# Kernel tuning notes

Measured on AMD Instinct MI355X. Metric: run time of the kernel, lower is better.

## Reference

```python
import jax, jax.numpy as jnp
import numpy as np

B, Tq, DIM = 4, 2048, 1024
TKV, N_LAT, DLAT = 16, 64, 1024
HEADS, DHEAD = 8, 64
LN_EPS = 1e-5


def setup_inputs() -> dict:
    key = jax.random.key(0)
    ks = jax.random.split(key, 6)
    qo = jax.random.normal(ks[0], (B, Tq, DIM), dtype=jnp.float32)
    kvo = jax.random.normal(ks[1], (B, TKV, N_LAT, DLAT), dtype=jnp.float32)
    # 16 media tokens, evenly spaced, first at index 16 (so q_time==0 for early tokens)
    media = jnp.zeros((B, Tq), dtype=bool)
    idx = 16 + jnp.arange(TKV) * (Tq // TKV)  # 16, 144, ..., 1936
    media = media.at[:, idx].set(True)
    ln_g = jnp.ones((DIM,), dtype=jnp.float32)
    ln_b = jnp.zeros((DIM,), dtype=jnp.float32)
    Wq = jax.random.normal(ks[2], (DIM, HEADS * DHEAD), dtype=jnp.float32) * 0.02
    Wkv = jax.random.normal(ks[3], (DLAT, HEADS * DHEAD * 2), dtype=jnp.float32) * 0.02
    Wout = jax.random.normal(ks[4], (HEADS * DHEAD, DIM), dtype=jnp.float32) * 0.02
    return {"qo": qo, "kvo": kvo, "media_locations": media,
            "ln_g": ln_g, "ln_b": ln_b, "Wq": Wq, "Wkv": Wkv, "Wout": Wout}


def _layernorm(x, g, b):
    mu = jnp.mean(x, axis=-1, keepdims=True)
    var = jnp.var(x, axis=-1, keepdims=True)
    return (x - mu) * jax.lax.rsqrt(var + LN_EPS) * g + b


def reference(qo, kvo, media_locations, ln_g, ln_b, Wq, Wkv, Wout):
    scale = DHEAD ** (-0.5)
    b, tq, _ = qo.shape
    _, tkv, n, _ = kvo.shape
    q = _layernorm(qo, ln_g, ln_b) @ Wq  # (b, tq, h*d)
    q = q.reshape(b, tq, HEADS, DHEAD).transpose(0, 2, 1, 3) * scale  # b h i d
    kv = kvo.reshape(b, tkv * n, -1) @ Wkv  # (b, j, 2*h*d)
    k, v = jnp.split(kv, 2, axis=-1)
    k = k.reshape(b, tkv * n, HEADS, DHEAD).transpose(0, 2, 1, 3)  # b h j d
    v = v.reshape(b, tkv * n, HEADS, DHEAD).transpose(0, 2, 1, 3)
    sim = jnp.einsum('bhid,bhjd->bhij', q, k)  # (b, h, tq, tkv*n)
    kv_time = jnp.repeat(jnp.arange(tkv) + 1, n)  # (tkv*n,)
    q_time = jnp.cumsum(media_locations.astype(jnp.int32), axis=-1)  # (b, tq)
    mask = q_time[:, None, :, None] == kv_time[None, None, None, :]  # only_attend_immediate
    neg = -jnp.finfo(sim.dtype).max
    sim = jnp.where(mask, sim, neg)
    attn = jax.nn.softmax(sim, axis=-1)
    attn = jnp.where((q_time == 0)[:, None, :, None], 0.0, attn)
    out = jnp.einsum('bhij,bhjd->bhid', attn, v)
    out = out.transpose(0, 2, 1, 3).reshape(b, tq, HEADS * DHEAD)
    return out @ Wout
```

## Files before the change

### kernel.cpp

```cpp
#include <hip/hip_runtime.h>
#include <cstdint>
#include <cstddef>

#define BB    4
#define TQ    2048
#define DIM   1024
#define TKV   16
#define NLAT  64
#define DLAT  1024
#define HEADS 8
#define DHEAD 64
#define LN_EPS 1e-5f
#define NKV   (TKV*NLAT)
#define HD    (HEADS*DHEAD)

typedef unsigned short u16;
typedef __bf16 bf16x8 __attribute__((ext_vector_type(8)));
typedef float  f32x4  __attribute__((ext_vector_type(4)));

__device__ __forceinline__ u16 f2bf(float f) {
    unsigned u = __builtin_bit_cast(unsigned, f);
    u += 0x7fffu + ((u >> 16) & 1u);
    return (u16)(u >> 16);
}
__device__ __forceinline__ void gl_lds16(const void* g, void* l) {
    __builtin_amdgcn_global_load_lds(
        (const __attribute__((address_space(1))) void*)g,
        (__attribute__((address_space(3))) void*)l, 16, 0, 0);
}

__device__ __forceinline__ void transpose_dev(const float* __restrict__ W,
                                              u16* __restrict__ Wt,
                                              int K, int N, int n0, int k0,
                                              float (*tile)[33]) {
    int t = threadIdx.x;
    int r = t >> 3, c4 = (t & 7) * 4;
    float4 v = *(const float4*)&W[(size_t)(k0 + r) * N + n0 + c4];
    tile[r][c4 + 0] = v.x; tile[r][c4 + 1] = v.y;
    tile[r][c4 + 2] = v.z; tile[r][c4 + 3] = v.w;
    __syncthreads();
    uint2 pk;
    pk.x = (unsigned)f2bf(tile[c4 + 0][r]) | ((unsigned)f2bf(tile[c4 + 1][r]) << 16);
    pk.y = (unsigned)f2bf(tile[c4 + 2][r]) | ((unsigned)f2bf(tile[c4 + 3][r]) << 16);
    *(uint2*)&Wt[(size_t)(n0 + r) * K + k0 + c4] = pk;
}

__global__ __launch_bounds__(256) void prep_k(
    const float* __restrict__ qo, const float* __restrict__ kvo,
    const uint8_t* __restrict__ media,
    const float* __restrict__ ln_g, const float* __restrict__ ln_b,
    const float* __restrict__ Wq, const float* __restrict__ Wkv,
    const float* __restrict__ Wout,
    int* __restrict__ qt, u16* __restrict__ Aq, u16* __restrict__ Akv,
    u16* __restrict__ Wqt, u16* __restrict__ Wkvt, u16* __restrict__ Woutt) {
    __shared__ int part[256];
    __shared__ int cnt_sh;
    __shared__ float sh[8];
    __shared__ float mu_s, rs_s;
    __shared__ float tile[32][33];
    int blk = blockIdx.x, t = threadIdx.x;

    if (blk < 4) {
        int b = blk;
        int c = 0;
        for (int i = 0; i < 32; ++i) c += (media[t * 32 + i] != 0);
        part[t] = c;
        __syncthreads();
        if (t == 0) { int s = 0; for (int i = 0; i < 256; ++i) s += part[i]; cnt_sh = s; }
        __syncthreads();
        bool is_u8 = (cnt_sh >= 48);
        int vals[8];
        for (int i = 0; i < 8; ++i) {
            int idx = t * 8 + i;
            int m;
            if (is_u8) m = (media[(size_t)b * TQ + idx] != 0) ? 1 : 0;
            else       m = (((const uint32_t*)media)[(size_t)b * TQ + idx] != 0u) ? 1 : 0;
            vals[i] = m;
        }
        int loc = 0;
        for (int i = 0; i < 8; ++i) loc += vals[i];
        __syncthreads();
        part[t] = loc;
        __syncthreads();
        int pre = 0;
        for (int i = 0; i < t; ++i) pre += part[i];
        int run = pre;
        for (int i = 0; i < 8; ++i) {
            run += vals[i];
            qt[(size_t)b * TQ + t * 8 + i] = run;
        }
    } else if (blk < 4 + BB * TQ) {
        int row = blk - 4;
        float4 v = *(const float4*)(qo + (size_t)row * DIM + t * 4);
        float s  = v.x + v.y + v.z + v.w;
        float ss = v.x * v.x + v.y * v.y + v.z * v.z + v.w * v.w;
        for (int off = 32; off; off >>= 1) { s += __shfl_down(s, off); ss += __shfl_down(ss, off); }
        if ((t & 63) == 0) { sh[(t >> 6) * 2] = s; sh[(t >> 6) * 2 + 1] = ss; }
        __syncthreads();
        if (t == 0) {
            float S  = sh[0] + sh[2] + sh[4] + sh[6];
            float SS = sh[1] + sh[3] + sh[5] + sh[7];
            float m  = S * (1.0f / DIM);
            mu_s = m;
            rs_s = rsqrtf(SS * (1.0f / DIM) - m * m + LN_EPS);
        }
        __syncthreads();
        float mu = mu_s, rs = rs_s;
        float4 gv = *(const float4*)(ln_g + t * 4);
        float4 bv = *(const float4*)(ln_b + t * 4);
        float a0 = (v.x - mu) * rs * gv.x + bv.x;
        float a1 = (v.y - mu) * rs * gv.y + bv.y;
        float a2 = (v.z - mu) * rs * gv.z + bv.z;
        float a3 = (v.w - mu) * rs * gv.w + bv.w;
        uint2 pk;
        pk.x = (unsigned)f2bf(a0) | ((unsigned)f2bf(a1) << 16);
        pk.y = (unsigned)f2bf(a2) | ((unsigned)f2bf(a3) << 16);
        *(uint2*)(Aq + (size_t)row * DIM + t * 4) = pk;
    } else if (blk < 4 + BB * TQ + 2048) {
        size_t i = (size_t)(blk - 4 - BB * TQ) * 256 + t;
        float4 a = ((const float4*)kvo)[i * 2];
        float4 b = ((const float4*)kvo)[i * 2 + 1];
        uint4 pk;
        pk.x = (unsigned)f2bf(a.x) | ((unsigned)f2bf(a.y) << 16);
        pk.y = (unsigned)f2bf(a.z) | ((unsigned)f2bf(a.w) << 16);
        pk.z = (unsigned)f2bf(b.x) | ((unsigned)f2bf(b.y) << 16);
        pk.w = (unsigned)f2bf(b.z) | ((unsigned)f2bf(b.w) << 16);
        ((uint4*)Akv)[i] = pk;
    } else if (blk < 10244 + 512) {
        int id = blk - 10244;
        transpose_dev(Wq, Wqt, DIM, HD, (id & 15) * 32, (id >> 4) * 32, tile);
    } else if (blk < 10756 + 1024) {
        int id = blk - 10756;
        transpose_dev(Wkv, Wkvt, DLAT, 2 * HD, (id & 31) * 32, (id >> 5) * 32, tile);
    } else {
        int id = blk - 11780;
        transpose_dev(Wout, Woutt, HD, DIM, (id & 31) * 32, (id >> 5) * 32, tile);
    }
}

template <typename CT>
__device__ __forceinline__ void gemm_body(const u16* __restrict__ A,
                                          const u16* __restrict__ Bt,
                                          CT* __restrict__ C,
                                          int M, int N, int K, float outscale,
                                          int bx, int by,
                                          u16* As0, u16* Bs0, u16* As1, u16* Bs1) {
    int t = threadIdx.x;
    int lane = t & 63, w = t >> 6;
    int wr = w >> 1, wc = w & 1;
    int fr = lane & 15, fg = lane >> 4;
    int row0 = by * 128, col0 = bx * 128;

    const u16* Ag = A  + (size_t)(row0 + (t >> 2)) * K + (t & 3) * 8;
    const u16* Bg = Bt + (size_t)(col0 + (t >> 2)) * K + (t & 3) * 8;
    size_t rstr = (size_t)64 * K;

    int aoff = (wr * 64 + fr) * 32 + fg * 8;
    int boff = (wc * 64 + fr) * 32 + fg * 8;

    f32x4 acc[4][4];
#pragma unroll
    for (int mi = 0; mi < 4; ++mi)
#pragma unroll
        for (int ni = 0; ni < 4; ++ni) acc[mi][ni] = (f32x4){0.f, 0.f, 0.f, 0.f};

    auto stage = [&](u16* Asb, u16* Bsb, int k0) {
        char* al = (char*)Asb + w * 1024;
        char* bl = (char*)Bsb + w * 1024;
        gl_lds16(Ag + k0,        al);
        gl_lds16(Ag + k0 + rstr, al + 4096);
        gl_lds16(Bg + k0,        bl);
        gl_lds16(Bg + k0 + rstr, bl + 4096);
    };
    auto compute = [&](const u16* Asb, const u16* Bsb) {
        bf16x8 af[4], bfv[4];
#pragma unroll
        for (int mi = 0; mi < 4; ++mi) af[mi]  = *(const bf16x8*)(Asb + aoff + mi * 512);
#pragma unroll
        for (int ni = 0; ni < 4; ++ni) bfv[ni] = *(const bf16x8*)(Bsb + boff + ni * 512);
#pragma unroll
        for (int mi = 0; mi < 4; ++mi)
#pragma unroll
            for (int ni = 0; ni < 4; ++ni)
                acc[mi][ni] = __builtin_amdgcn_mfma_f32_16x16x32_bf16(
                    af[mi], bfv[ni], acc[mi][ni], 0, 0, 0);
    };

    int nt = K >> 5;
    stage(As0, Bs0, 0);
    __syncthreads();
    for (int it = 0; it < nt; it += 2) {
        stage(As1, Bs1, (it + 1) << 5);
        compute(As0, Bs0);
        __syncthreads();
        if (it + 2 < nt) stage(As0, Bs0, (it + 2) << 5);
        compute(As1, Bs1);
        __syncthreads();
    }

#pragma unroll
    for (int mi = 0; mi < 4; ++mi) {
        int r0 = row0 + wr * 64 + mi * 16 + fg * 4;
#pragma unroll
        for (int ni = 0; ni < 4; ++ni) {
            int c = col0 + wc * 64 + ni * 16 + fr;
#pragma unroll
            for (int j = 0; j < 4; ++j) {
                float val = acc[mi][ni][j] * outscale;
                if constexpr (sizeof(CT) == 2) C[(size_t)(r0 + j) * N + c] = f2bf(val);
                else                           C[(size_t)(r0 + j) * N + c] = val;
            }
        }
    }
}

__global__ __launch_bounds__(256) void proj_k(
    const u16* __restrict__ Aq,  const u16* __restrict__ Wqt,  u16* __restrict__ qb,
    const u16* __restrict__ Akv, const u16* __restrict__ Wkvt, u16* __restrict__ kvb) {
    __shared__ u16 As0[4096], Bs0[4096], As1[4096], Bs1[4096];
    int id = blockIdx.x;
    if (id < 256) {
        gemm_body<u16>(Aq, Wqt, qb, BB * TQ, HD, DIM, 0.125f, id & 3, id >> 2,
                       As0, Bs0, As1, Bs1);
    } else {
        id -= 256;
        gemm_body<u16>(Akv, Wkvt, kvb, BB * NKV, 2 * HD, DLAT, 1.0f, id & 7, id >> 3,
                       As0, Bs0, As1, Bs1);
    }
}

__global__ __launch_bounds__(256) void out_k(
    const u16* __restrict__ aob, const u16* __restrict__ Woutt, float* __restrict__ out) {
    __shared__ u16 As0[4096], Bs0[4096], As1[4096], Bs1[4096];
    int id = blockIdx.x;
    gemm_body<float>(aob, Woutt, out, BB * TQ, DIM, HD, 1.0f, id & 7, id >> 3,
                     As0, Bs0, As1, Bs1);
}

__global__ __launch_bounds__(256) void attn_k(
    const u16* __restrict__ q,
    const u16* __restrict__ kv,
    const int* __restrict__ qt,
    u16* __restrict__ ao) {
    __shared__ u16 Ks[4096];
    __shared__ u16 VT[4096];
    __shared__ u16 Ps[1024];
    __shared__ float redm[4][16], reds[4][16];
    int i0 = blockIdx.x * 16;
    int h  = blockIdx.y;
    int b  = blockIdx.z;
    int t  = threadIdx.x;
    int lane = t & 63, w = t >> 6;
    int fr = lane & 15, fg = lane >> 4;

    int t0 = qt[(size_t)b * TQ + i0];
    if (t0 == 0) {
        int row = t >> 4, c = (t & 15) * 4;
        *(uint2*)&ao[((size_t)(b * TQ + i0 + row)) * HD + h * DHEAD + c] = make_uint2(0, 0);
        return;
    }
    int j0 = (t0 - 1) * 64;

    {
        int j = t >> 2, c16 = (t & 3) * 16;
        const u16* kvrow = kv + ((size_t)(b * NKV + j0 + j)) * (2 * HD) + h * DHEAD;
        uint4 k0v = *(const uint4*)(kvrow + c16);
        uint4 k1v = *(const uint4*)(kvrow + c16 + 8);
        uint4 v0v = *(const uint4*)(kvrow + HD + c16);
        uint4 v1v = *(const uint4*)(kvrow + HD + c16 + 8);
        int kb = j * 128 + c16 * 2;
        int swz = (j & 7) << 4;
        *(uint4*)((char*)Ks + ((kb)      ^ swz)) = k0v;
        *(uint4*)((char*)Ks + ((kb + 16) ^ swz)) = k1v;
        const u16* ve0 = (const u16*)&v0v;
        const u16* ve1 = (const u16*)&v1v;
#pragma unroll
        for (int e = 0; e < 8; ++e) {
            int d0 = c16 + e, d1 = c16 + 8 + e;
            *(u16*)((char*)VT + ((d0 * 128 + j * 2) ^ ((d0 & 7) << 4))) = ve0[e];
            *(u16*)((char*)VT + ((d1 * 128 + j * 2) ^ ((d1 & 7) << 4))) = ve1[e];
        }
    }
    const u16* qrow = q + ((size_t)(b * TQ + i0 + fr)) * HD + h * DHEAD + fg * 8;
    bf16x8 aq0 = *(const bf16x8*)(qrow);
    bf16x8 aq1 = *(const bf16x8*)(qrow + 32);
    __syncthreads();

    int r = w * 16 + fr;
    bf16x8 bk0 = *(const bf16x8*)((char*)Ks + ((r * 128 + fg * 16)      ^ ((r & 7) << 4)));
    bf16x8 bk1 = *(const bf16x8*)((char*)Ks + ((r * 128 + 64 + fg * 16) ^ ((r & 7) << 4)));
    f32x4 s = (f32x4){0.f, 0.f, 0.f, 0.f};
    s = __builtin_amdgcn_mfma_f32_16x16x32_bf16(aq0, bk0, s, 0, 0, 0);
    s = __builtin_amdgcn_mfma_f32_16x16x32_bf16(aq1, bk1, s, 0, 0, 0);

    float mx[4];
#pragma unroll
    for (int j = 0; j < 4; ++j) {
        float m = s[j];
        for (int off = 1; off < 16; off <<= 1) m = fmaxf(m, __shfl_xor(m, off));
        mx[j] = m;
        redm[w][fg * 4 + j] = m;
    }
    __syncthreads();
    float p[4];
#pragma unroll
    for (int j = 0; j < 4; ++j) {
        int row = fg * 4 + j;
        float M = fmaxf(fmaxf(redm[0][row], redm[1][row]), fmaxf(redm[2][row], redm[3][row]));
        p[j] = __expf(s[j] - M);
        float sm = p[j];
        for (int off = 1; off < 16; off <<= 1) sm += __shfl_xor(sm, off);
        reds[w][row] = sm;
    }
    __syncthreads();
#pragma unroll
    for (int j = 0; j < 4; ++j) {
        int row = fg * 4 + j;
        float S = reds[0][row] + reds[1][row] + reds[2][row] + reds[3][row];
        u16 pb = f2bf(p[j] / S);
        *(u16*)((char*)Ps + ((row * 128 + (w * 16 + fr) * 2) ^ ((row & 7) << 4))) = pb;
    }
    __syncthreads();

    bf16x8 pa0 = *(const bf16x8*)((char*)Ps + ((fr * 128 + fg * 16)      ^ ((fr & 7) << 4)));
    bf16x8 pa1 = *(const bf16x8*)((char*)Ps + ((fr * 128 + 64 + fg * 16) ^ ((fr & 7) << 4)));
    int d = w * 16 + fr;
    bf16x8 bv0 = *(const bf16x8*)((char*)VT + ((d * 128 + fg * 16)      ^ ((d & 7) << 4)));
    bf16x8 bv1 = *(const bf16x8*)((char*)VT + ((d * 128 + 64 + fg * 16) ^ ((d & 7) << 4)));
    f32x4 o = (f32x4){0.f, 0.f, 0.f, 0.f};
    o = __builtin_amdgcn_mfma_f32_16x16x32_bf16(pa0, bv0, o, 0, 0, 0);
    o = __builtin_amdgcn_mfma_f32_16x16x32_bf16(pa1, bv1, o, 0, 0, 0);
#pragma unroll
    for (int j = 0; j < 4; ++j)
        ao[((size_t)(b * TQ + i0 + fg * 4 + j)) * HD + h * DHEAD + d] = f2bf(o[j]);
}

extern "C" void kernel_launch(void* const* d_in, const int* in_sizes, int n_in,
                              void* d_out, int out_size, void* d_ws, size_t ws_size,
                              hipStream_t stream) {
    const float*   qo    = (const float*)d_in[0];
    const float*   kvo   = (const float*)d_in[1];
    const uint8_t* media = (const uint8_t*)d_in[2];
    const float*   ln_g  = (const float*)d_in[3];
    const float*   ln_b  = (const float*)d_in[4];
    const float*   Wq    = (const float*)d_in[5];
    const float*   Wkv   = (const float*)d_in[6];
    const float*   Wout  = (const float*)d_in[7];
    float* out = (float*)d_out;

    char* ws = (char*)d_ws;
    const size_t MB = 1u << 20;
    int* qt    = (int*)(ws);
    u16* Aq    = (u16*)(ws + 1  * MB);
    u16* aob   = (u16*)(ws + 1  * MB);
    u16* Akv   = (u16*)(ws + 17 * MB);
    u16* Wqt   = (u16*)(ws + 25 * MB);
    u16* Wkvt  = (u16*)(ws + 26 * MB);
    u16* Woutt = (u16*)(ws + 28 * MB);
    u16* qb    = (u16*)(ws + 29 * MB);
    u16* kvb   = (u16*)(ws + 37 * MB);

    prep_k<<<dim3(12292), dim3(256), 0, stream>>>(qo, kvo, media, ln_g, ln_b,
                                                  Wq, Wkv, Wout,
                                                  qt, Aq, Akv, Wqt, Wkvt, Woutt);
    proj_k<<<dim3(512), dim3(256), 0, stream>>>(Aq, Wqt, qb, Akv, Wkvt, kvb);
    attn_k<<<dim3(TQ / 16, HEADS, BB), dim3(256), 0, stream>>>(qb, kvb, qt, aob);
    out_k<<<dim3(512), dim3(256), 0, stream>>>(aob, Woutt, out);
}
```

Measured before the change: 169.8 us.

## Pre-swizzle GEMM operands in global memory and widen K-tile to 64

The producers of the GEMM operands (LN output, kvo bf16 copy, transposed weights, attention output) now write each row in 16-byte chunks XOR-swizzled by row. The GEMM can then copy a 64-wide K tile straight into LDS with global_load_lds and read it without bank conflicts. The K step doubles, so each barrier pair covers twice the MFMA work and LDS use doubles to 64KB per block. The cost is coupling every producer to the swizzle layout and lower occupancy from the larger LDS footprint.

```diff
diff --git a/kernel.cpp b/kernel.cpp
--- a/kernel.cpp
+++ b/kernel.cpp
@@ -28,6 +28,9 @@
         (const __attribute__((address_space(1))) void*)g,
         (__attribute__((address_space(3))) void*)l, 16, 0, 0);
 }
+__device__ __forceinline__ int swz_idx(int col, int row) {
+    return (col & ~63) | ((((col >> 3) & 7) ^ (row & 7)) << 3) | (col & 7);
+}
 
 __device__ __forceinline__ void transpose_dev(const float* __restrict__ W,
                                               u16* __restrict__ Wt,
@@ -42,7 +45,8 @@
     uint2 pk;
     pk.x = (unsigned)f2bf(tile[c4 + 0][r]) | ((unsigned)f2bf(tile[c4 + 1][r]) << 16);
     pk.y = (unsigned)f2bf(tile[c4 + 2][r]) | ((unsigned)f2bf(tile[c4 + 3][r]) << 16);
-    *(uint2*)&Wt[(size_t)(n0 + r) * K + k0 + c4] = pk;
+    int n = n0 + r, k = k0 + c4;
+    *(uint2*)&Wt[(size_t)n * K + swz_idx(k, n)] = pk;
 }
 
 __global__ __launch_bounds__(256) void prep_k(
@@ -115,7 +119,7 @@
         uint2 pk;
         pk.x = (unsigned)f2bf(a0) | ((unsigned)f2bf(a1) << 16);
         pk.y = (unsigned)f2bf(a2) | ((unsigned)f2bf(a3) << 16);
-        *(uint2*)(Aq + (size_t)row * DIM + t * 4) = pk;
+        *(uint2*)(Aq + (size_t)row * DIM + swz_idx(t * 4, row)) = pk;
     } else if (blk < 4 + BB * TQ + 2048) {
         size_t i = (size_t)(blk - 4 - BB * TQ) * 256 + t;
         float4 a = ((const float4*)kvo)[i * 2];
@@ -125,7 +129,9 @@
         pk.y = (unsigned)f2bf(a.z) | ((unsigned)f2bf(a.w) << 16);
         pk.z = (unsigned)f2bf(b.x) | ((unsigned)f2bf(b.y) << 16);
         pk.w = (unsigned)f2bf(b.z) | ((unsigned)f2bf(b.w) << 16);
-        ((uint4*)Akv)[i] = pk;
+        int row = (int)(i >> 7);
+        size_t di = (i & ~(size_t)7) | (size_t)(((int)i & 7) ^ (row & 7));
+        ((uint4*)Akv)[di] = pk;
     } else if (blk < 10244 + 512) {
         int id = blk - 10244;
         transpose_dev(Wq, Wqt, DIM, HD, (id & 15) * 32, (id >> 4) * 32, tile);
@@ -139,9 +145,7 @@
 }
 
 template <typename CT>
-__device__ __forceinline__ void gemm_body(const u16* __restrict__ A,
-                                          const u16* __restrict__ Bt,
-                                          CT* __restrict__ C,
+__device__ __forceinline__ void gemm_body(const u16* A, const u16* Bt, CT* C,
                                           int M, int N, int K, float outscale,
                                           int bx, int by,
                                           u16* As0, u16* Bs0, u16* As1, u16* Bs1) {
@@ -150,13 +154,11 @@
     int wr = w >> 1, wc = w & 1;
     int fr = lane & 15, fg = lane >> 4;
     int row0 = by * 128, col0 = bx * 128;
-
-    const u16* Ag = A  + (size_t)(row0 + (t >> 2)) * K + (t & 3) * 8;
-    const u16* Bg = Bt + (size_t)(col0 + (t >> 2)) * K + (t & 3) * 8;
-    size_t rstr = (size_t)64 * K;
-
-    int aoff = (wr * 64 + fr) * 32 + fg * 8;
-    int boff = (wc * 64 + fr) * 32 + fg * 8;
+    int swz = fr & 7;
+
+    const u16* Ag = A  + (size_t)(row0 + w * 32 + (lane >> 3)) * K + (lane & 7) * 8;
+    const u16* Bg = Bt + (size_t)(col0 + w * 32 + (lane >> 3)) * K + (lane & 7) * 8;
+    size_t i8K = (size_t)8 * K;
 
     f32x4 acc[4][4];
 #pragma unroll
@@ -164,36 +166,43 @@
 #pragma unroll
         for (int ni = 0; ni < 4; ++ni) acc[mi][ni] = (f32x4){0.f, 0.f, 0.f, 0.f};
 
-    auto stage = [&](u16* Asb, u16* Bsb, int k0) {
-        char* al = (char*)Asb + w * 1024;
-        char* bl = (char*)Bsb + w * 1024;
-        gl_lds16(Ag + k0,        al);
-        gl_lds16(Ag + k0 + rstr, al + 4096);
-        gl_lds16(Bg + k0,        bl);
-        gl_lds16(Bg + k0 + rstr, bl + 4096);
+    auto stage = [&](u16* Asb, u16* Bsb, int kt) {
+        int k0 = kt << 6;
+#pragma unroll
+        for (int q = 0; q < 4; ++q) {
+            gl_lds16(Ag + k0 + q * i8K, (char*)Asb + w * 4096 + q * 1024);
+            gl_lds16(Bg + k0 + q * i8K, (char*)Bsb + w * 4096 + q * 1024);
+        }
     };
     auto compute = [&](const u16* Asb, const u16* Bsb) {
-        bf16x8 af[4], bfv[4];
-#pragma unroll
-        for (int mi = 0; mi < 4; ++mi) af[mi]  = *(const bf16x8*)(Asb + aoff + mi * 512);
-#pragma unroll
-        for (int ni = 0; ni < 4; ++ni) bfv[ni] = *(const bf16x8*)(Bsb + boff + ni * 512);
-#pragma unroll
-        for (int mi = 0; mi < 4; ++mi)
+#pragma unroll
+        for (int ks = 0; ks < 2; ++ks) {
+            bf16x8 af[4], bfv[4];
+#pragma unroll
+            for (int mi = 0; mi < 4; ++mi)
+                af[mi] = *(const bf16x8*)((const char*)Asb +
+                    (wr * 64 + mi * 16 + fr) * 128 + (((ks * 4 + fg) ^ swz) << 4));
 #pragma unroll
             for (int ni = 0; ni < 4; ++ni)
-                acc[mi][ni] = __builtin_amdgcn_mfma_f32_16x16x32_bf16(
-                    af[mi], bfv[ni], acc[mi][ni], 0, 0, 0);
+                bfv[ni] = *(const bf16x8*)((const char*)Bsb +
+                    (wc * 64 + ni * 16 + fr) * 128 + (((ks * 4 + fg) ^ swz) << 4));
+#pragma unroll
+            for (int mi = 0; mi < 4; ++mi)
+#pragma unroll
+                for (int ni = 0; ni < 4; ++ni)
+                    acc[mi][ni] = __builtin_amdgcn_mfma_f32_16x16x32_bf16(
+                        af[mi], bfv[ni], acc[mi][ni], 0, 0, 0);
+        }
     };
 
-    int nt = K >> 5;
+    int nt = K >> 6;
     stage(As0, Bs0, 0);
     __syncthreads();
-    for (int it = 0; it < nt; it += 2) {
-        stage(As1, Bs1, (it + 1) << 5);
+    for (int kt = 0; kt < nt; kt += 2) {
+        stage(As1, Bs1, kt + 1);
         compute(As0, Bs0);
         __syncthreads();
-        if (it + 2 < nt) stage(As0, Bs0, (it + 2) << 5);
+        if (kt + 2 < nt) stage(As0, Bs0, kt + 2);
         compute(As1, Bs1);
         __syncthreads();
     }
@@ -217,7 +226,7 @@
 __global__ __launch_bounds__(256) void proj_k(
     const u16* __restrict__ Aq,  const u16* __restrict__ Wqt,  u16* __restrict__ qb,
     const u16* __restrict__ Akv, const u16* __restrict__ Wkvt, u16* __restrict__ kvb) {
-    __shared__ u16 As0[4096], Bs0[4096], As1[4096], Bs1[4096];
+    __shared__ u16 As0[8192], Bs0[8192], As1[8192], Bs1[8192];
     int id = blockIdx.x;
     if (id < 256) {
         gemm_body<u16>(Aq, Wqt, qb, BB * TQ, HD, DIM, 0.125f, id & 3, id >> 2,
@@ -231,7 +240,7 @@
 
 __global__ __launch_bounds__(256) void out_k(
     const u16* __restrict__ aob, const u16* __restrict__ Woutt, float* __restrict__ out) {
-    __shared__ u16 As0[4096], Bs0[4096], As1[4096], Bs1[4096];
+    __shared__ u16 As0[8192], Bs0[8192], As1[8192], Bs1[8192];
     int id = blockIdx.x;
     gemm_body<float>(aob, Woutt, out, BB * TQ, DIM, HD, 1.0f, id & 7, id >> 3,
                      As0, Bs0, As1, Bs1);
@@ -255,8 +264,8 @@
 
     int t0 = qt[(size_t)b * TQ + i0];
     if (t0 == 0) {
-        int row = t >> 4, c = (t & 15) * 4;
-        *(uint2*)&ao[((size_t)(b * TQ + i0 + row)) * HD + h * DHEAD + c] = make_uint2(0, 0);
+        int row = i0 + (t >> 4), cc = h * DHEAD + (t & 15) * 4;
+        *(uint2*)&ao[((size_t)(b * TQ + row)) * HD + swz_idx(cc, row)] = make_uint2(0, 0);
         return;
     }
     int j0 = (t0 - 1) * 64;
@@ -269,9 +278,9 @@
         uint4 v0v = *(const uint4*)(kvrow + HD + c16);
         uint4 v1v = *(const uint4*)(kvrow + HD + c16 + 8);
         int kb = j * 128 + c16 * 2;
-        int swz = (j & 7) << 4;
-        *(uint4*)((char*)Ks + ((kb)      ^ swz)) = k0v;
-        *(uint4*)((char*)Ks + ((kb + 16) ^ swz)) = k1v;
+        int sw = (j & 7) << 4;
+        *(uint4*)((char*)Ks + ((kb)      ^ sw)) = k0v;
+        *(uint4*)((char*)Ks + ((kb + 16) ^ sw)) = k1v;
         const u16* ve0 = (const u16*)&v0v;
         const u16* ve1 = (const u16*)&v1v;
 #pragma unroll
@@ -293,12 +302,10 @@
     s = __builtin_amdgcn_mfma_f32_16x16x32_bf16(aq0, bk0, s, 0, 0, 0);
     s = __builtin_amdgcn_mfma_f32_16x16x32_bf16(aq1, bk1, s, 0, 0, 0);
 
-    float mx[4];
 #pragma unroll
     for (int j = 0; j < 4; ++j) {
         float m = s[j];
         for (int off = 1; off < 16; off <<= 1) m = fmaxf(m, __shfl_xor(m, off));
-        mx[j] = m;
         redm[w][fg * 4 + j] = m;
     }
     __syncthreads();
@@ -330,9 +337,12 @@
     f32x4 o = (f32x4){0.f, 0.f, 0.f, 0.f};
     o = __builtin_amdgcn_mfma_f32_16x16x32_bf16(pa0, bv0, o, 0, 0, 0);
     o = __builtin_amdgcn_mfma_f32_16x16x32_bf16(pa1, bv1, o, 0, 0, 0);
-#pragma unroll
-    for (int j = 0; j < 4; ++j)
-        ao[((size_t)(b * TQ + i0 + fg * 4 + j)) * HD + h * DHEAD + d] = f2bf(o[j]);
+    int cc = h * DHEAD + d;
+#pragma unroll
+    for (int j = 0; j < 4; ++j) {
+        int row = i0 + fg * 4 + j;
+        ao[((size_t)(b * TQ + row)) * HD + swz_idx(cc, row)] = f2bf(o[j]);
+    }
 }
 
 extern "C" void kernel_launch(void* const* d_in, const int* in_sizes, int n_in,
```

Result: no change. 166.9 us (-1.7%).
